# Optimization experiments

Hardware: AMD Instinct MI355X
Metric: run time of the kernel (lower is better)

The kernel has to match this reference:

```python
import jax, jax.numpy as jnp
import numpy as np

DIM = 512        # token feature dim
HID = 1024       # expert hidden dim (dim * 2)
E = 16           # num_experts
N = 8192         # num tokens
TOPK = 2         # experts active per token (routing sparsity)


def setup_inputs() -> dict:
    key = jax.random.key(0)
    k_x, k_s, k_w1, k_w2 = jax.random.split(key, 4)
    x = jax.random.normal(k_x, (N, DIM), dtype=jnp.float32)
    # sparse routing scores: top-2 experts per token get nonzero score, rest 0
    scores = jax.random.uniform(k_s, (N, E), dtype=jnp.float32)
    vals, idx = jax.lax.top_k(scores, TOPK)
    routing_tensor = jnp.zeros((N, E), jnp.float32).at[jnp.arange(N)[:, None], idx].set(vals)
    # per-expert MLP params (depth=2, bias=True): Linear(DIM->HID), GELU, Linear(HID->DIM)
    W1 = jax.random.normal(k_w1, (E, DIM, HID), dtype=jnp.float32) * (1.0 / np.sqrt(DIM))
    b1 = jnp.zeros((E, HID), jnp.float32)
    W2 = jax.random.normal(k_w2, (E, HID, DIM), dtype=jnp.float32) * (1.0 / np.sqrt(HID))
    b2 = jnp.zeros((E, DIM), jnp.float32)
    return {"x": x, "routing_tensor": routing_tensor, "W1": W1, "b1": b1, "W2": W2, "b2": b2}


def reference(x, routing_tensor, W1, b1, W2, b2):
    # out[n] = sum_e routing[n,e] * MLP_e(x[n]); rows with score 0 contribute 0,
    # which is exactly the original mask-gather / scatter-add semantics.
    h = jax.nn.gelu(jnp.einsum('nd,edh->enh', x, W1) + b1[:, None, :], approximate=False)
    y = jnp.einsum('enh,ehd->end', h, W2) + b2[:, None, :]  # [E, N, DIM]
    return jnp.einsum('end,ne->nd', y, routing_tensor)       # combine weighted by scores
```

## Files before the change

### kernel.cpp

```cpp
#include <hip/hip_runtime.h>
#include <hip/hip_bf16.h>

#define NTOK 8192
#define DIM 512
#define HID 1024
#define NE 16
#define CAP 1280

typedef __attribute__((ext_vector_type(8))) short short8;
typedef __attribute__((ext_vector_type(4))) float f32x4;

static __device__ __forceinline__ unsigned short f2bf(float f) {
    __hip_bfloat16 h = __float2bfloat16(f);
    return __builtin_bit_cast(unsigned short, h);
}

static __device__ __forceinline__ void gl_lds16(const unsigned short* g, unsigned short* l) {
    __builtin_amdgcn_global_load_lds(
        (const __attribute__((address_space(1))) unsigned int*)g,
        (__attribute__((address_space(3))) unsigned int*)l, 16, 0, 0);
}

static __device__ __forceinline__ float gelu_f(float v) {
    float u = v * (0.7978845608f + 0.0356774081f * v * v);
    return v / (1.0f + __expf(-2.0f * u));
}

__global__ void transpose_cvt2(const float* __restrict__ W1, const float* __restrict__ W2,
                               unsigned short* __restrict__ w1t, unsigned short* __restrict__ w2t) {
    __shared__ float tile[32][33];
    int b = blockIdx.x;
    const float* src; unsigned short* dst; int R, C, bx, by;
    if (b < 8192) {
        int e = b >> 9, rem = b & 511; bx = rem & 31; by = rem >> 5;
        R = DIM; C = HID;
        src = W1 + (size_t)e * R * C; dst = w1t + (size_t)e * R * C;
    } else {
        int bb = b - 8192;
        int e = bb >> 9, rem = bb & 511; bx = rem & 15; by = rem >> 4;
        R = HID; C = DIM;
        src = W2 + (size_t)e * R * C; dst = w2t + (size_t)e * R * C;
    }
    int c0 = bx * 32, r0 = by * 32;
    int tx = threadIdx.x, ty = threadIdx.y;
    #pragma unroll
    for (int i = 0; i < 32; i += 8)
        tile[ty + i][tx] = src[(size_t)(r0 + ty + i) * C + c0 + tx];
    __syncthreads();
    #pragma unroll
    for (int i = 0; i < 32; i += 8)
        dst[(size_t)(c0 + ty + i) * R + r0 + tx] = f2bf(tile[tx][ty + i]);
}

__global__ __launch_bounds__(256) void route_fill(const float* __restrict__ routing,
                                                  int* __restrict__ cnt,
                                                  int* __restrict__ sidx,
                                                  float* __restrict__ wtb) {
    __shared__ int lcnt[NE], lbase[NE];
    int t = threadIdx.x;
    int n = blockIdx.x * 256 + t;
    if (t < NE) lcnt[t] = 0;
    __syncthreads();
    int mye[2]; float myw[2]; int mypos[2]; int slot = 0;
    #pragma unroll
    for (int e = 0; e < NE; e++) {
        float r = routing[n * NE + e];
        if (r != 0.0f && slot < 2) {
            mye[slot] = e; myw[slot] = r;
            mypos[slot] = atomicAdd(&lcnt[e], 1);
            slot++;
        }
    }
    __syncthreads();
    if (t < NE) lbase[t] = atomicAdd(&cnt[t], lcnt[t]);
    __syncthreads();
    for (int s = 0; s < slot; s++) {
        int e = mye[s];
        int p = lbase[e] + mypos[s];
        if (p < CAP) { sidx[e * CAP + p] = n * 2 + s; wtb[e * CAP + p] = myw[s]; }
    }
}

__global__ void gather_x(const float* __restrict__ x, const int* __restrict__ cnt,
                         const int* __restrict__ sidx, unsigned short* __restrict__ xg) {
    int b = blockIdx.x;
    int e = b / CAP, row = b - e * CAP;
    int t = threadIdx.x;
    int c = cnt[e]; c = c > CAP ? CAP : c;
    ushort4 o;
    if (row < c) {
        int n = sidx[b] >> 1;
        float4 v = ((const float4*)(x + (size_t)n * DIM))[t];
        o.x = f2bf(v.x); o.y = f2bf(v.y); o.z = f2bf(v.z); o.w = f2bf(v.w);
    } else {
        o.x = 0; o.y = 0; o.z = 0; o.w = 0;
    }
    ((ushort4*)(xg + (size_t)b * DIM))[t] = o;
}

template <int K>
__device__ __forceinline__ void mfma_main(const unsigned short* __restrict__ A,
                                          const unsigned short* __restrict__ B,
                                          unsigned short* As, unsigned short* Bs,
                                          f32x4 acc[4][4]) {
    int t = threadIdx.x;
    int wave = t >> 6, lane = t & 63;
    int wm = wave >> 1, wn = wave & 1;
    int quad = lane >> 4, l16 = lane & 15;
    int lr = lane >> 3;
    int col = (lane & 7) << 3;
    for (int kc = 0; kc < K; kc += 64) {
        __syncthreads();
        #pragma unroll
        for (int j = 0; j < 4; j++) {
            int rb = wave * 32 + j * 8;
            gl_lds16(A + (size_t)(rb + lr) * K + kc + col, As + rb * 64);
            gl_lds16(B + (size_t)(rb + lr) * K + kc + col, Bs + rb * 64);
        }
        __syncthreads();
        #pragma unroll
        for (int kk = 0; kk < 64; kk += 32) {
            short8 av[4], bv[4];
            #pragma unroll
            for (int mt = 0; mt < 4; mt++)
                av[mt] = *(const short8*)(&As[(wm * 64 + mt * 16 + l16) * 64 + kk + quad * 8]);
            #pragma unroll
            for (int nt = 0; nt < 4; nt++)
                bv[nt] = *(const short8*)(&Bs[(wn * 64 + nt * 16 + l16) * 64 + kk + quad * 8]);
            #pragma unroll
            for (int mt = 0; mt < 4; mt++)
                #pragma unroll
                for (int nt = 0; nt < 4; nt++)
                    acc[mt][nt] = __builtin_amdgcn_mfma_f32_16x16x32_bf16(
                        av[mt], bv[nt], acc[mt][nt], 0, 0, 0);
        }
    }
}

template <int K>
__device__ __forceinline__ void mfma_main_db(const unsigned short* __restrict__ A,
                                             const unsigned short* __restrict__ B,
                                             unsigned short (*As)[128 * 64],
                                             unsigned short (*Bs)[128 * 64],
                                             f32x4 acc[4][4]) {
    int t = threadIdx.x;
    int wave = t >> 6, lane = t & 63;
    int wm = wave >> 1, wn = wave & 1;
    int quad = lane >> 4, l16 = lane & 15;
    int lr = lane >> 3;
    int col = (lane & 7) << 3;
    #pragma unroll
    for (int j = 0; j < 4; j++) {
        int rb = wave * 32 + j * 8;
        gl_lds16(A + (size_t)(rb + lr) * K + col, As[0] + rb * 64);
        gl_lds16(B + (size_t)(rb + lr) * K + col, Bs[0] + rb * 64);
    }
    __syncthreads();
    int cur = 0;
    for (int kc = 64; kc <= K; kc += 64) {
        if (kc < K) {
            #pragma unroll
            for (int j = 0; j < 4; j++) {
                int rb = wave * 32 + j * 8;
                gl_lds16(A + (size_t)(rb + lr) * K + kc + col, As[cur ^ 1] + rb * 64);
                gl_lds16(B + (size_t)(rb + lr) * K + kc + col, Bs[cur ^ 1] + rb * 64);
            }
        }
        #pragma unroll
        for (int kk = 0; kk < 64; kk += 32) {
            short8 av[4], bv[4];
            #pragma unroll
            for (int mt = 0; mt < 4; mt++)
                av[mt] = *(const short8*)(&As[cur][(wm * 64 + mt * 16 + l16) * 64 + kk + quad * 8]);
            #pragma unroll
            for (int nt = 0; nt < 4; nt++)
                bv[nt] = *(const short8*)(&Bs[cur][(wn * 64 + nt * 16 + l16) * 64 + kk + quad * 8]);
            #pragma unroll
            for (int mt = 0; mt < 4; mt++)
                #pragma unroll
                for (int nt = 0; nt < 4; nt++)
                    acc[mt][nt] = __builtin_amdgcn_mfma_f32_16x16x32_bf16(
                        av[mt], bv[nt], acc[mt][nt], 0, 0, 0);
        }
        __syncthreads();
        cur ^= 1;
    }
}

__global__ __launch_bounds__(256) void gemm1_gelu(
    const unsigned short* __restrict__ xg, const unsigned short* __restrict__ w1t,
    const float* __restrict__ b1, const int* __restrict__ cnt,
    unsigned short* __restrict__ hbuf) {
    __shared__ __align__(16) unsigned short As[128 * 64];
    __shared__ __align__(16) unsigned short Bs[128 * 64];
    int e = blockIdx.z;
    int c = cnt[e]; c = c > CAP ? CAP : c;
    int m0 = blockIdx.y * 128;
    if (m0 >= c) return;
    int n0 = blockIdx.x * 128;
    const unsigned short* A = xg + ((size_t)e * CAP + m0) * DIM;
    const unsigned short* B = w1t + ((size_t)e * HID + n0) * DIM;
    f32x4 z = {0.f, 0.f, 0.f, 0.f};
    f32x4 acc[4][4];
    #pragma unroll
    for (int mt = 0; mt < 4; mt++)
        #pragma unroll
        for (int nt = 0; nt < 4; nt++) acc[mt][nt] = z;
    mfma_main<DIM>(A, B, As, Bs, acc);
    int t = threadIdx.x;
    int wave = t >> 6, lane = t & 63;
    int wm = wave >> 1, wn = wave & 1, quad = lane >> 4, l16 = lane & 15;
    #pragma unroll
    for (int nt = 0; nt < 4; nt++) {
        int gn = n0 + wn * 64 + nt * 16 + l16;
        float bias = b1[e * HID + gn];
        #pragma unroll
        for (int mt = 0; mt < 4; mt++) {
            #pragma unroll
            for (int r = 0; r < 4; r++) {
                int gm = m0 + wm * 64 + mt * 16 + quad * 4 + r;
                float v = acc[mt][nt][r] + bias;
                hbuf[((size_t)e * CAP + gm) * HID + gn] = f2bf(gelu_f(v));
            }
        }
    }
}

__global__ __launch_bounds__(256) void gemm2_store(
    const unsigned short* __restrict__ hbuf, const unsigned short* __restrict__ w2t,
    const float* __restrict__ b2, const int* __restrict__ cnt,
    const int* __restrict__ sidx, const float* __restrict__ wtb,
    float* __restrict__ ybuf) {
    __shared__ __align__(16) unsigned short As[2][128 * 64];
    __shared__ __align__(16) unsigned short Bs[2][128 * 64];
    int e = blockIdx.z;
    int c = cnt[e]; c = c > CAP ? CAP : c;
    int m0 = blockIdx.y * 128;
    if (m0 >= c) return;
    int n0 = blockIdx.x * 128;
    const unsigned short* A = hbuf + ((size_t)e * CAP + m0) * HID;
    const unsigned short* B = w2t + ((size_t)e * DIM + n0) * HID;
    f32x4 z = {0.f, 0.f, 0.f, 0.f};
    f32x4 acc[4][4];
    #pragma unroll
    for (int mt = 0; mt < 4; mt++)
        #pragma unroll
        for (int nt = 0; nt < 4; nt++) acc[mt][nt] = z;
    mfma_main_db<HID>(A, B, As, Bs, acc);
    int t = threadIdx.x;
    int wave = t >> 6, lane = t & 63;
    int wm = wave >> 1, wn = wave & 1, quad = lane >> 4, l16 = lane & 15;
    #pragma unroll
    for (int mt = 0; mt < 4; mt++) {
        #pragma unroll
        for (int r = 0; r < 4; r++) {
            int gm = m0 + wm * 64 + mt * 16 + quad * 4 + r;
            if (gm < c) {
                int si = sidx[e * CAP + gm];
                float wgt = wtb[e * CAP + gm];
                float* yrow = ybuf + (size_t)si * DIM;
                #pragma unroll
                for (int nt = 0; nt < 4; nt++) {
                    int gn = n0 + wn * 64 + nt * 16 + l16;
                    yrow[gn] = wgt * (acc[mt][nt][r] + b2[e * DIM + gn]);
                }
            }
        }
    }
}

__global__ void combine(const float* __restrict__ yb, float* __restrict__ out) {
    int i = blockIdx.x * 256 + threadIdx.x;
    int n = i >> 7, d4 = i & 127;
    float4 a = ((const float4*)(yb + (size_t)(2 * n) * DIM))[d4];
    float4 b = ((const float4*)(yb + (size_t)(2 * n + 1) * DIM))[d4];
    float4 o;
    o.x = a.x + b.x; o.y = a.y + b.y; o.z = a.z + b.z; o.w = a.w + b.w;
    ((float4*)(out + (size_t)n * DIM))[d4] = o;
}

extern "C" void kernel_launch(void* const* d_in, const int* in_sizes, int n_in,
                              void* d_out, int out_size, void* d_ws, size_t ws_size,
                              hipStream_t stream) {
    const float* x       = (const float*)d_in[0];
    const float* routing = (const float*)d_in[1];
    const float* W1      = (const float*)d_in[2];
    const float* b1      = (const float*)d_in[3];
    const float* W2      = (const float*)d_in[4];
    const float* b2      = (const float*)d_in[5];
    float* out = (float*)d_out;

    char* w = (char*)d_ws;
    int*   cnt  = (int*)w;
    int*   sidx = (int*)(w + 256);
    float* wtb  = (float*)(w + 256 + NE * CAP * 4);
    char* base = w + 256 + NE * CAP * 8;
    unsigned short* xg  = (unsigned short*)base;
    unsigned short* hb  = xg + (size_t)NE * CAP * DIM;
    unsigned short* w1t = hb + (size_t)NE * CAP * HID;
    unsigned short* w2t = w1t + (size_t)NE * HID * DIM;
    float* ybuf = (float*)(w2t + (size_t)NE * DIM * HID);

    hipMemsetAsync(cnt, 0, 256, stream);

    transpose_cvt2<<<16384, dim3(32, 8), 0, stream>>>(W1, W2, w1t, w2t);

    route_fill<<<NTOK / 256, 256, 0, stream>>>(routing, cnt, sidx, wtb);
    gather_x<<<NE * CAP, 128, 0, stream>>>(x, cnt, sidx, xg);

    gemm1_gelu<<<dim3(HID / 128, CAP / 128, NE), 256, 0, stream>>>(xg, w1t, b1, cnt, hb);
    gemm2_store<<<dim3(DIM / 128, CAP / 128, NE), 256, 0, stream>>>(hb, w2t, b2, cnt, sidx, wtb, ybuf);
    combine<<<(NTOK * DIM / 4) / 256, 256, 0, stream>>>(ybuf, out);
}
```

Measured before the change: 254.2 us.

## Shrink expert GEMM M-tile to 64 rows with grouped flat block ordering

Both expert GEMMs now use 64x128 tiles instead of 128x128, so each expert's padded capacity splits into 20 M-tiles. Blocks are launched on a flat grid with a swizzled order that groups 8 M-tiles per group sharing the same N tile, aiming for better L2 reuse of weights. GEMM2 also drops its LDS double buffering for the single-buffer loop, and both kernels get an occupancy hint of 5 blocks per CU. The smaller tiles should waste less work on partially filled tiles and spread more blocks across CUs, at the price of lower MFMA reuse per LDS load and more reloads of the weight tiles.

```diff
diff --git a/kernel.cpp b/kernel.cpp
--- a/kernel.cpp
+++ b/kernel.cpp
@@ -6,6 +6,7 @@
 #define HID 1024
 #define NE 16
 #define CAP 1280
+#define MT 20
 
 typedef __attribute__((ext_vector_type(8))) short short8;
 typedef __attribute__((ext_vector_type(4))) float f32x4;
@@ -99,10 +100,10 @@
 }
 
 template <int K>
-__device__ __forceinline__ void mfma_main(const unsigned short* __restrict__ A,
-                                          const unsigned short* __restrict__ B,
-                                          unsigned short* As, unsigned short* Bs,
-                                          f32x4 acc[4][4]) {
+__device__ __forceinline__ void mfma_main64(const unsigned short* __restrict__ A,
+                                            const unsigned short* __restrict__ B,
+                                            unsigned short* As, unsigned short* Bs,
+                                            f32x4 acc[2][4]) {
     int t = threadIdx.x;
     int wave = t >> 6, lane = t & 63;
     int wm = wave >> 1, wn = wave & 1;
@@ -112,23 +113,27 @@
     for (int kc = 0; kc < K; kc += 64) {
         __syncthreads();
         #pragma unroll
+        for (int j = 0; j < 2; j++) {
+            int rb = wave * 16 + j * 8;
+            gl_lds16(A + (size_t)(rb + lr) * K + kc + col, As + rb * 64);
+        }
+        #pragma unroll
         for (int j = 0; j < 4; j++) {
             int rb = wave * 32 + j * 8;
-            gl_lds16(A + (size_t)(rb + lr) * K + kc + col, As + rb * 64);
             gl_lds16(B + (size_t)(rb + lr) * K + kc + col, Bs + rb * 64);
         }
         __syncthreads();
         #pragma unroll
         for (int kk = 0; kk < 64; kk += 32) {
-            short8 av[4], bv[4];
-            #pragma unroll
-            for (int mt = 0; mt < 4; mt++)
-                av[mt] = *(const short8*)(&As[(wm * 64 + mt * 16 + l16) * 64 + kk + quad * 8]);
+            short8 av[2], bv[4];
+            #pragma unroll
+            for (int mt = 0; mt < 2; mt++)
+                av[mt] = *(const short8*)(&As[(wm * 32 + mt * 16 + l16) * 64 + kk + quad * 8]);
             #pragma unroll
             for (int nt = 0; nt < 4; nt++)
                 bv[nt] = *(const short8*)(&Bs[(wn * 64 + nt * 16 + l16) * 64 + kk + quad * 8]);
             #pragma unroll
-            for (int mt = 0; mt < 4; mt++)
+            for (int mt = 0; mt < 2; mt++)
                 #pragma unroll
                 for (int nt = 0; nt < 4; nt++)
                     acc[mt][nt] = __builtin_amdgcn_mfma_f32_16x16x32_bf16(
@@ -137,76 +142,30 @@
     }
 }
 
-template <int K>
-__device__ __forceinline__ void mfma_main_db(const unsigned short* __restrict__ A,
-                                             const unsigned short* __restrict__ B,
-                                             unsigned short (*As)[128 * 64],
-                                             unsigned short (*Bs)[128 * 64],
-                                             f32x4 acc[4][4]) {
-    int t = threadIdx.x;
-    int wave = t >> 6, lane = t & 63;
-    int wm = wave >> 1, wn = wave & 1;
-    int quad = lane >> 4, l16 = lane & 15;
-    int lr = lane >> 3;
-    int col = (lane & 7) << 3;
-    #pragma unroll
-    for (int j = 0; j < 4; j++) {
-        int rb = wave * 32 + j * 8;
-        gl_lds16(A + (size_t)(rb + lr) * K + col, As[0] + rb * 64);
-        gl_lds16(B + (size_t)(rb + lr) * K + col, Bs[0] + rb * 64);
-    }
-    __syncthreads();
-    int cur = 0;
-    for (int kc = 64; kc <= K; kc += 64) {
-        if (kc < K) {
-            #pragma unroll
-            for (int j = 0; j < 4; j++) {
-                int rb = wave * 32 + j * 8;
-                gl_lds16(A + (size_t)(rb + lr) * K + kc + col, As[cur ^ 1] + rb * 64);
-                gl_lds16(B + (size_t)(rb + lr) * K + kc + col, Bs[cur ^ 1] + rb * 64);
-            }
-        }
-        #pragma unroll
-        for (int kk = 0; kk < 64; kk += 32) {
-            short8 av[4], bv[4];
-            #pragma unroll
-            for (int mt = 0; mt < 4; mt++)
-                av[mt] = *(const short8*)(&As[cur][(wm * 64 + mt * 16 + l16) * 64 + kk + quad * 8]);
-            #pragma unroll
-            for (int nt = 0; nt < 4; nt++)
-                bv[nt] = *(const short8*)(&Bs[cur][(wn * 64 + nt * 16 + l16) * 64 + kk + quad * 8]);
-            #pragma unroll
-            for (int mt = 0; mt < 4; mt++)
-                #pragma unroll
-                for (int nt = 0; nt < 4; nt++)
-                    acc[mt][nt] = __builtin_amdgcn_mfma_f32_16x16x32_bf16(
-                        av[mt], bv[nt], acc[mt][nt], 0, 0, 0);
-        }
-        __syncthreads();
-        cur ^= 1;
-    }
-}
-
-__global__ __launch_bounds__(256) void gemm1_gelu(
+
+__global__ __launch_bounds__(256, 5) void gemm1_gelu(
     const unsigned short* __restrict__ xg, const unsigned short* __restrict__ w1t,
     const float* __restrict__ b1, const int* __restrict__ cnt,
     unsigned short* __restrict__ hbuf) {
-    __shared__ __align__(16) unsigned short As[128 * 64];
+    __shared__ __align__(16) unsigned short As[64 * 64];
     __shared__ __align__(16) unsigned short Bs[128 * 64];
-    int e = blockIdx.z;
+    int L = blockIdx.x;
+    int cc = L & 7, n = (L >> 3) & 7, g = L >> 6;
+    int pi = cc + (g << 3);
+    int e = pi / MT, m = pi % MT;
     int c = cnt[e]; c = c > CAP ? CAP : c;
-    int m0 = blockIdx.y * 128;
+    int m0 = m * 64;
     if (m0 >= c) return;
-    int n0 = blockIdx.x * 128;
+    int n0 = n * 128;
     const unsigned short* A = xg + ((size_t)e * CAP + m0) * DIM;
     const unsigned short* B = w1t + ((size_t)e * HID + n0) * DIM;
     f32x4 z = {0.f, 0.f, 0.f, 0.f};
-    f32x4 acc[4][4];
-    #pragma unroll
-    for (int mt = 0; mt < 4; mt++)
+    f32x4 acc[2][4];
+    #pragma unroll
+    for (int mt = 0; mt < 2; mt++)
         #pragma unroll
         for (int nt = 0; nt < 4; nt++) acc[mt][nt] = z;
-    mfma_main<DIM>(A, B, As, Bs, acc);
+    mfma_main64<DIM>(A, B, As, Bs, acc);
     int t = threadIdx.x;
     int wave = t >> 6, lane = t & 63;
     int wm = wave >> 1, wn = wave & 1, quad = lane >> 4, l16 = lane & 15;
@@ -215,10 +174,10 @@
         int gn = n0 + wn * 64 + nt * 16 + l16;
         float bias = b1[e * HID + gn];
         #pragma unroll
-        for (int mt = 0; mt < 4; mt++) {
+        for (int mt = 0; mt < 2; mt++) {
             #pragma unroll
             for (int r = 0; r < 4; r++) {
-                int gm = m0 + wm * 64 + mt * 16 + quad * 4 + r;
+                int gm = m0 + wm * 32 + mt * 16 + quad * 4 + r;
                 float v = acc[mt][nt][r] + bias;
                 hbuf[((size_t)e * CAP + gm) * HID + gn] = f2bf(gelu_f(v));
             }
@@ -226,35 +185,38 @@
     }
 }
 
-__global__ __launch_bounds__(256) void gemm2_store(
+__global__ __launch_bounds__(256, 5) void gemm2_store(
     const unsigned short* __restrict__ hbuf, const unsigned short* __restrict__ w2t,
     const float* __restrict__ b2, const int* __restrict__ cnt,
     const int* __restrict__ sidx, const float* __restrict__ wtb,
     float* __restrict__ ybuf) {
-    __shared__ __align__(16) unsigned short As[2][128 * 64];
-    __shared__ __align__(16) unsigned short Bs[2][128 * 64];
-    int e = blockIdx.z;
+    __shared__ __align__(16) unsigned short As[64 * 64];
+    __shared__ __align__(16) unsigned short Bs[128 * 64];
+    int L = blockIdx.x;
+    int cc = L & 7, n = (L >> 3) & 3, g = L >> 5;
+    int pi = cc + (g << 3);
+    int e = pi / MT, m = pi % MT;
     int c = cnt[e]; c = c > CAP ? CAP : c;
-    int m0 = blockIdx.y * 128;
+    int m0 = m * 64;
     if (m0 >= c) return;
-    int n0 = blockIdx.x * 128;
+    int n0 = n * 128;
     const unsigned short* A = hbuf + ((size_t)e * CAP + m0) * HID;
     const unsigned short* B = w2t + ((size_t)e * DIM + n0) * HID;
     f32x4 z = {0.f, 0.f, 0.f, 0.f};
-    f32x4 acc[4][4];
-    #pragma unroll
-    for (int mt = 0; mt < 4; mt++)
+    f32x4 acc[2][4];
+    #pragma unroll
+    for (int mt = 0; mt < 2; mt++)
         #pragma unroll
         for (int nt = 0; nt < 4; nt++) acc[mt][nt] = z;
-    mfma_main_db<HID>(A, B, As, Bs, acc);
+    mfma_main64<HID>(A, B, As, Bs, acc);
     int t = threadIdx.x;
     int wave = t >> 6, lane = t & 63;
     int wm = wave >> 1, wn = wave & 1, quad = lane >> 4, l16 = lane & 15;
     #pragma unroll
-    for (int mt = 0; mt < 4; mt++) {
+    for (int mt = 0; mt < 2; mt++) {
         #pragma unroll
         for (int r = 0; r < 4; r++) {
-            int gm = m0 + wm * 64 + mt * 16 + quad * 4 + r;
+            int gm = m0 + wm * 32 + mt * 16 + quad * 4 + r;
             if (gm < c) {
                 int si = sidx[e * CAP + gm];
                 float wgt = wtb[e * CAP + gm];
@@ -308,7 +270,7 @@
     route_fill<<<NTOK / 256, 256, 0, stream>>>(routing, cnt, sidx, wtb);
     gather_x<<<NE * CAP, 128, 0, stream>>>(x, cnt, sidx, xg);
 
-    gemm1_gelu<<<dim3(HID / 128, CAP / 128, NE), 256, 0, stream>>>(xg, w1t, b1, cnt, hb);
-    gemm2_store<<<dim3(DIM / 128, CAP / 128, NE), 256, 0, stream>>>(hb, w2t, b2, cnt, sidx, wtb, ybuf);
+    gemm1_gelu<<<8 * MT * NE, 256, 0, stream>>>(xg, w1t, b1, cnt, hb);
+    gemm2_store<<<4 * MT * NE, 256, 0, stream>>>(hb, w2t, b2, cnt, sidx, wtb, ybuf);
     combine<<<(NTOK * DIM / 4) / 256, 256, 0, stream>>>(ybuf, out);
 }
```

Measured after the change: 226.8 us. 1.12x faster.
